# Kernel optimization log

Measured on AMD Instinct MI355X. Metric: run time of the kernel, lower is better.

Reference implementation:

```python
import jax, jax.numpy as jnp
import numpy as np

N = 100000        # nodes
E = 1600000       # edges
D = 128           # feature dim (all layers)
G = 128           # graphs
C = 10            # num_classes
L = 3             # conv layers
EPS = 1e-5
SLOPE = 0.03


def setup_inputs() -> dict:
    key = jax.random.key(0)
    ks = jax.random.split(key, 12)
    x = jax.random.normal(ks[0], (N, D), dtype=jnp.float32)
    edge_index = jax.random.randint(ks[1], (2, E), 0, N, dtype=jnp.int64)
    batch = jnp.sort(jax.random.randint(ks[2], (N,), 0, G, dtype=jnp.int64))
    s = 1.0 / np.sqrt(D)
    Wc = jax.random.uniform(ks[3], (L, D, D), jnp.float32, -s, s)
    bc = jax.random.uniform(ks[4], (L, D), jnp.float32, -s, s)
    bn_gamma = jnp.ones((2, D), jnp.float32)
    bn_beta = jnp.zeros((2, D), jnp.float32)
    bn_mean = jax.random.normal(ks[5], (2, D), jnp.float32) * 0.1
    bn_var = jax.random.uniform(ks[6], (2, D), jnp.float32, 0.5, 1.5)
    lin_w = jax.random.uniform(ks[7], (C, D), jnp.float32, -s, s)
    lin_b = jax.random.uniform(ks[8], (C,), jnp.float32, -s, s)
    return {"x": x, "edge_index": edge_index, "batch": batch, "Wc": Wc,
            "bc": bc, "bn_gamma": bn_gamma, "bn_beta": bn_beta,
            "bn_mean": bn_mean, "bn_var": bn_var, "lin_w": lin_w, "lin_b": lin_b}


def _gcn_norm(edge_index):
    # add self-loops, compute D^{-1/2}[row] * D^{-1/2}[col] (PyG gcn_norm)
    loops = jnp.arange(N, dtype=edge_index.dtype)
    row = jnp.concatenate([edge_index[0], loops])
    col = jnp.concatenate([edge_index[1], loops])
    deg = jax.ops.segment_sum(jnp.ones_like(col, dtype=jnp.float32), col, num_segments=N)
    dis = jnp.where(deg > 0, jax.lax.rsqrt(deg), 0.0)
    return row, col, dis[row] * dis[col]


def reference(x, edge_index, batch, Wc, bc, bn_gamma, bn_beta, bn_mean, bn_var, lin_w, lin_b):
    row, col, norm = _gcn_norm(edge_index)
    h = x
    for i in range(L):
        h = h @ Wc[i]                                          # linear transform [N, D]
        msg = h[row] * norm[:, None]                           # gather + normalize [E+N, D]
        h = jax.ops.segment_sum(msg, col, num_segments=N) + bc[i]
        if i < 2:  # batchnorm only for i < len(batchnorms)-1 (eval mode, running stats)
            h = (h - bn_mean[i]) * jax.lax.rsqrt(bn_var[i] + EPS) * bn_gamma[i] + bn_beta[i]
        h = jnp.where(h > 0, h, SLOPE * h)                     # LeakyReLU(0.03)
    # global mean pool over graphs
    counts = jax.ops.segment_sum(jnp.ones((N,), jnp.float32), batch, num_segments=G)
    pooled = jax.ops.segment_sum(h, batch, num_segments=G) / jnp.maximum(counts, 1.0)[:, None]
    # dropout is identity in eval; final linear head
    return pooled @ lin_w.T + lin_b                            # [G, C]
```

## Files before the change

kernel.cpp:

```cpp
#include <hip/hip_runtime.h>
#include <hip/hip_bf16.h>

#define NN 100000
#define EE 1600000
#define DD 128
#define GG 128
#define CC 10
#define NPB 256
#define NB 391
#define SCAP 5120
#define VPT 16
#define CPAD 32
#define PPN 64

typedef __attribute__((ext_vector_type(8))) short bf16x8;
typedef __attribute__((ext_vector_type(4))) float f32x4;
typedef __attribute__((ext_vector_type(2))) float f32x2;
typedef unsigned int u32;

__device__ inline float blo(u32 u) { return __uint_as_float(u << 16); }
__device__ inline float bhi(u32 u) { return __uint_as_float(u & 0xffff0000u); }
__device__ inline u32 bpack(float x, float y) {
    u32 bx = __float_as_uint(x);
    u32 by = __float_as_uint(y);
    bx = (bx + 0x7fffu + ((bx >> 16) & 1u)) >> 16;
    by = (by + 0x7fffu + ((by >> 16) & 1u)) & 0xffff0000u;
    return bx | by;
}

__global__ __launch_bounds__(256) void k_bcount(const int* __restrict__ col,
                                                int* __restrict__ bhist) {
    __shared__ int lh[NB];
    int tid = threadIdx.x;
    for (int b = tid; b < NB; b += 256) lh[b] = 0;
    __syncthreads();
    int base = blockIdx.x * (256 * VPT);
#pragma unroll
    for (int j = 0; j < VPT; j++) {
        int e = base + j * 256 + tid;
        if (e < EE) atomicAdd(&lh[col[e] >> 8], 1);
    }
    __syncthreads();
    for (int b = tid; b < NB; b += 256) {
        int h = lh[b];
        if (h) atomicAdd(&bhist[b * CPAD], h);
    }
}

__global__ __launch_bounds__(512) void k_bscan(const int* __restrict__ bhist,
                                               int* __restrict__ boffs,
                                               int* __restrict__ bcur) {
    __shared__ int s[512];
    int tid = threadIdx.x;
    int c = (tid < NB) ? bhist[tid * CPAD] : 0;
    s[tid] = c;
    __syncthreads();
    for (int off = 1; off < 512; off <<= 1) {
        int v = (tid >= off) ? s[tid - off] : 0;
        __syncthreads();
        s[tid] += v;
        __syncthreads();
    }
    int excl = s[tid] - c;
    if (tid < NB) {
        boffs[tid] = excl;
        bcur[tid * CPAD] = excl;
    }
    if (tid == NB - 1) boffs[NB] = excl + c;
}

__global__ __launch_bounds__(256) void k_part(const int* __restrict__ row, const int* __restrict__ col,
                                              int* __restrict__ bcur, u32* __restrict__ pairs) {
    __shared__ int lhist[NB];
    __shared__ int gbase[NB];
    __shared__ int lcur[NB];
    int tid = threadIdx.x;
    for (int b = tid; b < NB; b += 256) lhist[b] = 0;
    __syncthreads();
    int base = blockIdx.x * (256 * VPT);
    u32 v[VPT];
    int bb[VPT];
#pragma unroll
    for (int j = 0; j < VPT; j++) {
        int e = base + j * 256 + tid;
        if (e < EE) {
            int r = row[e], c = col[e];
            v[j] = ((u32)r << 8) | (u32)(c & 255);
            bb[j] = c >> 8;
            atomicAdd(&lhist[bb[j]], 1);
        } else {
            bb[j] = -1;
        }
    }
    __syncthreads();
    for (int b = tid; b < NB; b += 256) {
        int h = lhist[b];
        gbase[b] = h ? atomicAdd(&bcur[b * CPAD], h) : 0;
        lcur[b] = 0;
    }
    __syncthreads();
#pragma unroll
    for (int j = 0; j < VPT; j++) {
        if (bb[j] >= 0) {
            int slot = gbase[bb[j]] + atomicAdd(&lcur[bb[j]], 1);
            pairs[slot] = v[j];
        }
    }
}

__global__ __launch_bounds__(256) void k_sort(const u32* __restrict__ pairs,
                                              const int* __restrict__ boffs,
                                              int* __restrict__ offs,
                                              float* __restrict__ dis,
                                              int* __restrict__ src) {
    int b = blockIdx.x;
    int tid = threadIdx.x;
    int nstart = b << 8;
    int nvalid = NN - nstart;
    if (nvalid > NPB) nvalid = NPB;
    int base = boffs[b];
    int eend = boffs[b + 1];
    int cnt = eend - base;
    __shared__ int lcnt[NPB];
    __shared__ int lscan[NPB];
    __shared__ int lcur[NPB];
    __shared__ int lsrc[SCAP];
    lcnt[tid] = 0;
    __syncthreads();
    for (int e = base + tid; e < eend; e += 256)
        atomicAdd(&lcnt[pairs[e] & 255u], 1);
    __syncthreads();
    int c = lcnt[tid];
    lscan[tid] = c;
    __syncthreads();
    for (int off = 1; off < 256; off <<= 1) {
        int v = (tid >= off) ? lscan[tid - off] : 0;
        __syncthreads();
        lscan[tid] += v;
        __syncthreads();
    }
    int excl = lscan[tid] - c;
    if (tid < nvalid) {
        offs[nstart + tid] = base + excl;
        dis[nstart + tid] = rsqrtf((float)(c + 1));
    }
    if (b == NB - 1 && tid == 255) offs[NN] = EE;
    lcur[tid] = excl;
    __syncthreads();
    if (cnt <= SCAP) {
        for (int e = base + tid; e < eend; e += 256) {
            u32 v = pairs[e];
            int slot = atomicAdd(&lcur[v & 255u], 1);
            lsrc[slot] = (int)(v >> 8);
        }
        __syncthreads();
        for (int i = tid; i < cnt; i += 256)
            src[base + i] = lsrc[i];
    } else {
        for (int e = base + tid; e < eend; e += 256) {
            u32 v = pairs[e];
            int slot = base + atomicAdd(&lcur[v & 255u], 1);
            src[slot] = (int)(v >> 8);
        }
    }
}

__global__ void k_prep(const float* __restrict__ Wc, const float* __restrict__ bc,
                       const float* __restrict__ gamma, const float* __restrict__ beta,
                       const float* __restrict__ mean, const float* __restrict__ var,
                       __hip_bfloat16* __restrict__ WT,
                       float* __restrict__ tc) {
    int i = blockIdx.x * 256 + threadIdx.x;
    if (i < 3 * 128) {
        int l = i >> 7, d = i & 127;
        float t;
        if (l < 2) {
            float s = gamma[l * 128 + d] * rsqrtf(var[l * 128 + d] + 1e-5f);
            t = (bc[l * 128 + d] - mean[l * 128 + d]) * s + beta[l * 128 + d];
        } else {
            t = bc[2 * 128 + d];
        }
        tc[i] = t;
    }
    if (i < 3 * 16384) {
        int l = i >> 14, r = (i >> 7) & 127, k = i & 127;
        float s = 1.f;
        if (l < 2) s = gamma[l * 128 + r] * rsqrtf(var[l * 128 + r] + 1e-5f);
        WT[i] = __float2bfloat16(Wc[l * 16384 + k * 128 + r] * s);
    }
}

template <int FP32IN>
__global__ __launch_bounds__(256) void k_gemm(const void* __restrict__ Ain,
                                              const __hip_bfloat16* __restrict__ WT,
                                              const float* __restrict__ dis,
                                              __hip_bfloat16* __restrict__ Cout) {
    int wave = threadIdx.x >> 6, lane = threadIdx.x & 63;
    int lg = lane >> 4, lr = lane & 15;
    int r0w = blockIdx.x * 64 + wave * 16;
    f32x4 zero = {0.f, 0.f, 0.f, 0.f};
    f32x4 acc[8];
#pragma unroll
    for (int ct = 0; ct < 8; ct++) acc[ct] = zero;

    int arow = r0w + lr;
    if (arow > NN - 1) arow = NN - 1;

#pragma unroll
    for (int kk = 0; kk < 4; kk++) {
        bf16x8 a;
        if (FP32IN) {
            const float* ap = (const float*)Ain + (size_t)arow * 128 + kk * 32 + lg * 8;
            float4 f0 = *(const float4*)ap;
            float4 f1 = *(const float4*)(ap + 4);
            u32 t0 = bpack(f0.x, f0.y), t1 = bpack(f0.z, f0.w);
            u32 t2 = bpack(f1.x, f1.y), t3 = bpack(f1.z, f1.w);
            uint4 t = make_uint4(t0, t1, t2, t3);
            a = *(bf16x8*)&t;
        } else {
            a = *(const bf16x8*)((const __hip_bfloat16*)Ain + (size_t)arow * 128 + kk * 32 + lg * 8);
        }
#pragma unroll
        for (int ct = 0; ct < 8; ct++) {
            bf16x8 b = *(const bf16x8*)(WT + (size_t)(ct * 16 + lr) * 128 + kk * 32 + lg * 8);
            acc[ct] = __builtin_amdgcn_mfma_f32_16x16x32_bf16(a, b, acc[ct], 0, 0, 0);
        }
    }
    float dv[4];
#pragma unroll
    for (int r = 0; r < 4; r++) {
        int row = r0w + lg * 4 + r;
        dv[r] = (row < NN) ? dis[row] : 0.f;
    }
#pragma unroll
    for (int ct = 0; ct < 8; ct++) {
#pragma unroll
        for (int r = 0; r < 4; r++) {
            int row = r0w + lg * 4 + r;
            if (row < NN) Cout[(size_t)row * 128 + ct * 16 + lr] = __float2bfloat16(acc[ct][r] * dv[r]);
        }
    }
}

__global__ __launch_bounds__(256) void k_agg(const u32* __restrict__ hin,
                                             const int* __restrict__ offs,
                                             const int* __restrict__ src,
                                             const float* __restrict__ dis,
                                             const float* __restrict__ tc,
                                             u32* __restrict__ hout) {
    int node = (blockIdx.x << 2) + (threadIdx.x >> 6);
    int lane = threadIdx.x & 63;
    if (node >= NN) return;
    int e0 = __builtin_amdgcn_readfirstlane(offs[node]);
    int e1 = __builtin_amdgcn_readfirstlane(offs[node + 1]);
    u32 self = hin[((u32)node << 6) + lane];
    f32x2 acc = {blo(self), bhi(self)};
    int e = e0;
    for (; e + 16 <= e1; e += 16) {
        u32 u[16];
#pragma unroll
        for (int j = 0; j < 16; j++) {
            u32 s = (u32)src[e + j];
            u[j] = hin[(s << 6) + lane];
        }
#pragma unroll
        for (int j = 0; j < 16; j++) {
            f32x2 v = {blo(u[j]), bhi(u[j])};
            acc += v;
        }
    }
    for (; e + 8 <= e1; e += 8) {
        u32 u[8];
#pragma unroll
        for (int j = 0; j < 8; j++) {
            u32 s = (u32)src[e + j];
            u[j] = hin[(s << 6) + lane];
        }
#pragma unroll
        for (int j = 0; j < 8; j++) {
            f32x2 v = {blo(u[j]), bhi(u[j])};
            acc += v;
        }
    }
    for (; e < e1; e++) {
        u32 u = hin[((u32)src[e] << 6) + lane];
        f32x2 v = {blo(u), bhi(u)};
        acc += v;
    }
    float dn = dis[node];
    int d0 = lane * 2;
    float r0 = acc.x * dn + tc[d0];
    float r1 = acc.y * dn + tc[d0 + 1];
    r0 = r0 > 0.f ? r0 : 0.03f * r0;
    r1 = r1 > 0.f ? r1 : 0.03f * r1;
    hout[((u32)node << 6) + lane] = bpack(r0, r1);
}

__global__ __launch_bounds__(64) void k_pool(const u32* __restrict__ h,
                                             const int* __restrict__ batch,
                                             float* __restrict__ pooled,
                                             float* __restrict__ counts) {
    int lane = threadIdx.x;
    int n0 = blockIdx.x * PPN;
    if (n0 >= NN) return;
    int n1 = n0 + PPN;
    if (n1 > NN) n1 = NN;
    float a0 = 0.f, a1 = 0.f, cnt = 0.f;
    int g = batch[n0];
    for (int n = n0; n < n1; n++) {
        int bg = batch[n];
        if (bg != g) {
            atomicAdd(&pooled[g * 128 + lane * 2], a0);
            atomicAdd(&pooled[g * 128 + lane * 2 + 1], a1);
            if (lane == 0) atomicAdd(&counts[g], cnt);
            a0 = 0.f; a1 = 0.f; cnt = 0.f; g = bg;
        }
        u32 u = h[(u32)n * 64u + lane];
        a0 += blo(u); a1 += bhi(u);
        cnt += 1.f;
    }
    atomicAdd(&pooled[g * 128 + lane * 2], a0);
    atomicAdd(&pooled[g * 128 + lane * 2 + 1], a1);
    if (lane == 0) atomicAdd(&counts[g], cnt);
}

__global__ void k_head(const float* __restrict__ pooled, const float* __restrict__ counts,
                       const float* __restrict__ w, const float* __restrict__ b,
                       float* __restrict__ out) {
    int i = blockIdx.x * blockDim.x + threadIdx.x;
    if (i >= GG * CC) return;
    int g = i / CC, c = i % CC;
    float cnt = counts[g];
    cnt = cnt > 1.f ? cnt : 1.f;
    float inv = 1.f / cnt;
    const float* p = &pooled[g * 128];
    const float* ww = &w[c * 128];
    float acc = 0.f;
    for (int d = 0; d < 128; d++) acc += p[d] * ww[d];
    out[i] = acc * inv + b[c];
}

extern "C" void kernel_launch(void* const* d_in, const int* in_sizes, int n_in,
                              void* d_out, int out_size, void* d_ws, size_t ws_size,
                              hipStream_t stream) {
    const float* x     = (const float*)d_in[0];
    const int*   ei    = (const int*)d_in[1];
    const int*   row   = ei;
    const int*   col   = ei + EE;
    const int*   batch = (const int*)d_in[2];
    const float* Wc    = (const float*)d_in[3];
    const float* bc    = (const float*)d_in[4];
    const float* gamma = (const float*)d_in[5];
    const float* beta  = (const float*)d_in[6];
    const float* mean  = (const float*)d_in[7];
    const float* var   = (const float*)d_in[8];
    const float* lw    = (const float*)d_in[9];
    const float* lb    = (const float*)d_in[10];
    float* out = (float*)d_out;

    char* p = (char*)d_ws;
    auto alloc = [&](size_t bytes) -> char* {
        char* r = p;
        p += (bytes + 255) & ~(size_t)255;
        return r;
    };
    float* dis    = (float*)alloc((size_t)NN * 4);
    int*   offs   = (int*)alloc((size_t)(NN + 1) * 4);
    int*   bhist  = (int*)alloc((size_t)NB * CPAD * 4);
    int*   boffs  = (int*)alloc((size_t)(NB + 1) * 4);
    int*   bcur   = (int*)alloc((size_t)NB * CPAD * 4);
    int*   src    = (int*)alloc((size_t)EE * 4);
    __hip_bfloat16* WT = (__hip_bfloat16*)alloc((size_t)3 * 16384 * 2);
    float* tc     = (float*)alloc((size_t)3 * 128 * 4);
    float* pooled = (float*)alloc((size_t)GG * 128 * 4);
    float* counts = (float*)alloc((size_t)GG * 4);
    __hip_bfloat16* h0b = (__hip_bfloat16*)alloc((size_t)NN * 128 * 2);
    __hip_bfloat16* h1b = (__hip_bfloat16*)alloc((size_t)NN * 128 * 2);
    u32* pairs = (u32*)h0b;

    hipMemsetAsync(bhist, 0, (size_t)NB * CPAD * 4, stream);
    hipMemsetAsync(pooled, 0, (size_t)GG * 128 * 4, stream);
    hipMemsetAsync(counts, 0, (size_t)GG * 4, stream);

    const int eb_grid = (EE + 256 * VPT - 1) / (256 * VPT);
    k_bcount<<<eb_grid, 256, 0, stream>>>(col, bhist);
    k_bscan<<<1, 512, 0, stream>>>(bhist, boffs, bcur);
    k_part<<<eb_grid, 256, 0, stream>>>(row, col, bcur, pairs);
    k_sort<<<NB, 256, 0, stream>>>(pairs, boffs, offs, dis, src);
    k_prep<<<192, 256, 0, stream>>>(Wc, bc, gamma, beta, mean, var, WT, tc);

    const int gemm_grid = (NN + 63) / 64;
    const int agg_grid  = (NN + 3) / 4;

    k_gemm<1><<<gemm_grid, 256, 0, stream>>>((const void*)x, WT, dis, h0b);
    k_agg<<<agg_grid, 256, 0, stream>>>((const u32*)h0b, offs, src, dis, tc, (u32*)h1b);
    k_gemm<0><<<gemm_grid, 256, 0, stream>>>((const void*)h1b, WT + 16384, dis, h0b);
    k_agg<<<agg_grid, 256, 0, stream>>>((const u32*)h0b, offs, src, dis, tc + 128, (u32*)h1b);
    k_gemm<0><<<gemm_grid, 256, 0, stream>>>((const void*)h1b, WT + 2 * 16384, dis, h0b);
    k_agg<<<agg_grid, 256, 0, stream>>>((const u32*)h0b, offs, src, dis, tc + 256, (u32*)h1b);

    k_pool<<<(NN + PPN - 1) / PPN, 64, 0, stream>>>((const u32*)h1b, batch, pooled, counts);
    k_head<<<(GG * CC + 255) / 256, 256, 0, stream>>>(pooled, counts, lw, lb, out);
}
```

Before: 397.5 us.

## Reorder GCN layer as aggregate-then-transform and fuse GEMM into aggregation kernel

Uses linearity to aggregate neighbour features first and then apply the weight matrix. Each 1024-thread block aggregates 16 nodes, stages them in shared memory and runs a 16x128 MFMA tile, which removes the separate GEMM kernels and their global round trips. The next layer's degree prescale is folded into the epilogue, and a small elementwise kernel converts the input to prescaled bf16. The cost is two block-wide barriers per 16 nodes, with half the waves idle during the MFMA, and large blocks that may hurt latency hiding for the irregular gathers.

Measured after the change: 379.9 us. 1.05x faster.

```diff
diff --git a/kernel.cpp b/kernel.cpp
--- a/kernel.cpp
+++ b/kernel.cpp
@@ -190,67 +190,30 @@
     }
 }
 
-template <int FP32IN>
-__global__ __launch_bounds__(256) void k_gemm(const void* __restrict__ Ain,
-                                              const __hip_bfloat16* __restrict__ WT,
-                                              const float* __restrict__ dis,
-                                              __hip_bfloat16* __restrict__ Cout) {
-    int wave = threadIdx.x >> 6, lane = threadIdx.x & 63;
-    int lg = lane >> 4, lr = lane & 15;
-    int r0w = blockIdx.x * 64 + wave * 16;
-    f32x4 zero = {0.f, 0.f, 0.f, 0.f};
-    f32x4 acc[8];
-#pragma unroll
-    for (int ct = 0; ct < 8; ct++) acc[ct] = zero;
-
-    int arow = r0w + lr;
-    if (arow > NN - 1) arow = NN - 1;
-
-#pragma unroll
-    for (int kk = 0; kk < 4; kk++) {
-        bf16x8 a;
-        if (FP32IN) {
-            const float* ap = (const float*)Ain + (size_t)arow * 128 + kk * 32 + lg * 8;
-            float4 f0 = *(const float4*)ap;
-            float4 f1 = *(const float4*)(ap + 4);
-            u32 t0 = bpack(f0.x, f0.y), t1 = bpack(f0.z, f0.w);
-            u32 t2 = bpack(f1.x, f1.y), t3 = bpack(f1.z, f1.w);
-            uint4 t = make_uint4(t0, t1, t2, t3);
-            a = *(bf16x8*)&t;
-        } else {
-            a = *(const bf16x8*)((const __hip_bfloat16*)Ain + (size_t)arow * 128 + kk * 32 + lg * 8);
-        }
-#pragma unroll
-        for (int ct = 0; ct < 8; ct++) {
-            bf16x8 b = *(const bf16x8*)(WT + (size_t)(ct * 16 + lr) * 128 + kk * 32 + lg * 8);
-            acc[ct] = __builtin_amdgcn_mfma_f32_16x16x32_bf16(a, b, acc[ct], 0, 0, 0);
-        }
-    }
-    float dv[4];
-#pragma unroll
-    for (int r = 0; r < 4; r++) {
-        int row = r0w + lg * 4 + r;
-        dv[r] = (row < NN) ? dis[row] : 0.f;
-    }
-#pragma unroll
-    for (int ct = 0; ct < 8; ct++) {
-#pragma unroll
-        for (int r = 0; r < 4; r++) {
-            int row = r0w + lg * 4 + r;
-            if (row < NN) Cout[(size_t)row * 128 + ct * 16 + lr] = __float2bfloat16(acc[ct][r] * dv[r]);
-        }
-    }
-}
-
-__global__ __launch_bounds__(256) void k_agg(const u32* __restrict__ hin,
-                                             const int* __restrict__ offs,
-                                             const int* __restrict__ src,
+__global__ __launch_bounds__(256) void k_pre(const float* __restrict__ x,
                                              const float* __restrict__ dis,
-                                             const float* __restrict__ tc,
-                                             u32* __restrict__ hout) {
-    int node = (blockIdx.x << 2) + (threadIdx.x >> 6);
+                                             u32* __restrict__ hs) {
+    int i = blockIdx.x * 256 + threadIdx.x;
+    if (i < NN * 64) {
+        float dn = dis[i >> 6];
+        float2 v = ((const float2*)x)[i];
+        hs[i] = bpack(v.x * dn, v.y * dn);
+    }
+}
+
+template <int PRESCALE>
+__global__ __launch_bounds__(1024) void k_aggT(const u32* __restrict__ hin,
+                                               const int* __restrict__ offs,
+                                               const int* __restrict__ src,
+                                               const float* __restrict__ dis,
+                                               const __hip_bfloat16* __restrict__ WT,
+                                               const float* __restrict__ tc,
+                                               u32* __restrict__ hout) {
+    __shared__ u32   Atile[16][68];
+    __shared__ float Otile[16][132];
+    int wid = threadIdx.x >> 6;
     int lane = threadIdx.x & 63;
-    if (node >= NN) return;
+    int node = blockIdx.x * 16 + wid;
     int e0 = __builtin_amdgcn_readfirstlane(offs[node]);
     int e1 = __builtin_amdgcn_readfirstlane(offs[node + 1]);
     u32 self = hin[((u32)node << 6) + lane];
@@ -288,11 +251,28 @@
         acc += v;
     }
     float dn = dis[node];
+    Atile[wid][lane] = bpack(acc.x * dn, acc.y * dn);
+    __syncthreads();
+    if (wid < 8) {
+        int lg = lane >> 4, lr = lane & 15;
+        f32x4 c4 = {0.f, 0.f, 0.f, 0.f};
+#pragma unroll
+        for (int kk = 0; kk < 4; kk++) {
+            bf16x8 a = *(const bf16x8*)&Atile[lr][kk * 16 + lg * 4];
+            bf16x8 b = *(const bf16x8*)(WT + (size_t)(wid * 16 + lr) * 128 + kk * 32 + lg * 8);
+            c4 = __builtin_amdgcn_mfma_f32_16x16x32_bf16(a, b, c4, 0, 0, 0);
+        }
+#pragma unroll
+        for (int r = 0; r < 4; r++)
+            Otile[lg * 4 + r][wid * 16 + lr] = c4[r];
+    }
+    __syncthreads();
     int d0 = lane * 2;
-    float r0 = acc.x * dn + tc[d0];
-    float r1 = acc.y * dn + tc[d0 + 1];
+    float r0 = Otile[wid][d0]     + tc[d0];
+    float r1 = Otile[wid][d0 + 1] + tc[d0 + 1];
     r0 = r0 > 0.f ? r0 : 0.03f * r0;
     r1 = r1 > 0.f ? r1 : 0.03f * r1;
+    if (PRESCALE) { r0 *= dn; r1 *= dn; }
     hout[((u32)node << 6) + lane] = bpack(r0, r1);
 }
 
@@ -388,16 +368,13 @@
     k_part<<<eb_grid, 256, 0, stream>>>(row, col, bcur, pairs);
     k_sort<<<NB, 256, 0, stream>>>(pairs, boffs, offs, dis, src);
     k_prep<<<192, 256, 0, stream>>>(Wc, bc, gamma, beta, mean, var, WT, tc);
-
-    const int gemm_grid = (NN + 63) / 64;
-    const int agg_grid  = (NN + 3) / 4;
-
-    k_gemm<1><<<gemm_grid, 256, 0, stream>>>((const void*)x, WT, dis, h0b);
-    k_agg<<<agg_grid, 256, 0, stream>>>((const u32*)h0b, offs, src, dis, tc, (u32*)h1b);
-    k_gemm<0><<<gemm_grid, 256, 0, stream>>>((const void*)h1b, WT + 16384, dis, h0b);
-    k_agg<<<agg_grid, 256, 0, stream>>>((const u32*)h0b, offs, src, dis, tc + 128, (u32*)h1b);
-    k_gemm<0><<<gemm_grid, 256, 0, stream>>>((const void*)h1b, WT + 2 * 16384, dis, h0b);
-    k_agg<<<agg_grid, 256, 0, stream>>>((const u32*)h0b, offs, src, dis, tc + 256, (u32*)h1b);
+    k_pre<<<(NN * 64 + 255) / 256, 256, 0, stream>>>(x, dis, (u32*)h0b);
+
+    const int fused_grid = NN / 16;
+
+    k_aggT<1><<<fused_grid, 1024, 0, stream>>>((const u32*)h0b, offs, src, dis, WT,           tc,       (u32*)h1b);
+    k_aggT<1><<<fused_grid, 1024, 0, stream>>>((const u32*)h1b, offs, src, dis, WT + 16384,   tc + 128, (u32*)h0b);
+    k_aggT<0><<<fused_grid, 1024, 0, stream>>>((const u32*)h0b, offs, src, dis, WT + 2*16384, tc + 256, (u32*)h1b);
 
     k_pool<<<(NN + PPN - 1) / PPN, 64, 0, stream>>>((const u32*)h1b, batch, pooled, counts);
     k_head<<<(GG * CC + 255) / 256, 256, 0, stream>>>(pooled, counts, lw, lb, out);
```
